# Optimization experiments

Hardware: AMD Instinct MI355X
Metric: run time of the kernel (lower is better)

The kernel has to match this reference:

```python
import jax, jax.numpy as jnp
import numpy as np

ROPE_THETA = 10000.0

def rope(x):
    # x: [B, H, T, D], D even. Standard rotate-half rotary embedding.
    T, D = x.shape[-2], x.shape[-1]
    half = D // 2
    inv_freq = 1.0 / (ROPE_THETA ** (jnp.arange(half, dtype=x.dtype) / half))
    ang = jnp.arange(T, dtype=x.dtype)[:, None] * inv_freq[None, :]  # [T, half]
    cos, sin = jnp.cos(ang), jnp.sin(ang)
    x1, x2 = x[..., :half], x[..., half:]
    return jnp.concatenate([x1 * cos - x2 * sin, x1 * sin + x2 * cos], axis=-1)


def setup_inputs() -> dict:
    key = jax.random.key(0)
    kq, kk, kv = jax.random.split(key, 3)
    shape = (2, 8, 4096, 64)  # [B, H, T, D]
    return {
        "Q": jax.random.normal(kq, shape, dtype=jnp.float32),
        "K": jax.random.normal(kk, shape, dtype=jnp.float32),
        "V": jax.random.normal(kv, shape, dtype=jnp.float32),
    }


def reference(Q, K, V):
    # Unnormalized causal linear attention with RoPE:
    #   tril(RoPE(Q) @ RoPE(K)^T, diagonal=-1) @ V
    Qr = rope(Q)
    Kr = rope(K)
    scores = jnp.einsum("bhqd,bhkd->bhqk", Qr, Kr)  # [B,H,T,T]
    T = scores.shape[-1]
    # strictly lower triangular (diagonal=-1): keep q_idx > k_idx
    mask = jnp.arange(T)[:, None] > jnp.arange(T)[None, :]
    scores = jnp.where(mask, scores, jnp.zeros((), dtype=scores.dtype))
    return jnp.einsum("bhqk,bhkd->bhqd", scores, V)
```

## Files before the change

kernel.cpp:

```cpp
#include <hip/hip_runtime.h>

#define G 16
#define T 4096
#define DD 64

typedef __attribute__((ext_vector_type(8))) short bf16x8;
typedef __attribute__((ext_vector_type(4))) short bf16x4;
typedef __attribute__((ext_vector_type(4))) float f32x4;
typedef unsigned short U16;

__device__ __forceinline__ float bf2f(U16 u) {
  union { unsigned int u; float f; } x; x.u = ((unsigned int)u) << 16; return x.f;
}
__device__ __forceinline__ U16 f2bf(float f) {
  union { float f; unsigned int u; } x; x.f = f;
  unsigned int r = x.u + 0x7FFFu + ((x.u >> 16) & 1u);
  return (U16)(r >> 16);
}

#define MFMA(a, b, c) __builtin_amdgcn_mfma_f32_16x16x32_bf16((a), (b), (c), 0, 0, 0)

#define ROPE_C 0.28782313662425575f

__global__ __launch_bounds__(256) void k_phase1(const float* __restrict__ K, const float* __restrict__ V,
                                                U16* __restrict__ Kr, U16* __restrict__ VbT,
                                                U16* __restrict__ Xu) {
  __shared__ __align__(16) U16 KrT[64][72];
  __shared__ __align__(16) U16 VT[64][72];
  int wid = blockIdx.x;
  int g = wid >> 6, b = wid & 63;
  int k0 = b * 64;
  int tid = threadIdx.x;

  int r = tid >> 2, qq = tid & 3, d0 = qq * 8;
  int t = k0 + r;
  size_t base = ((size_t)g * T + t) * DD;

  {
    const float* rp = K + base;
    float x1[8], x2[8];
    *(float4*)&x1[0] = *(const float4*)(rp + d0);
    *(float4*)&x1[4] = *(const float4*)(rp + d0 + 4);
    *(float4*)&x2[0] = *(const float4*)(rp + d0 + 32);
    *(float4*)&x2[4] = *(const float4*)(rp + d0 + 36);
    bf16x8 v1, v2;
#pragma unroll
    for (int i = 0; i < 8; ++i) {
      float invf = __expf(-(float)(d0 + i) * ROPE_C);
      float ang = (float)t * invf;
      float s, c;
      __sincosf(ang, &s, &c);
      float o1 = x1[i] * c - x2[i] * s;
      float o2 = x1[i] * s + x2[i] * c;
      U16 b1 = f2bf(o1), b2 = f2bf(o2);
      v1[i] = (short)b1; v2[i] = (short)b2;
      KrT[d0 + i][r]      = b1;
      KrT[d0 + i + 32][r] = b2;
    }
    *(bf16x8*)(Kr + base + d0)      = v1;
    *(bf16x8*)(Kr + base + d0 + 32) = v2;
  }
  {
    const float* vp = V + base;
    float y1[8], y2[8];
    *(float4*)&y1[0] = *(const float4*)(vp + d0);
    *(float4*)&y1[4] = *(const float4*)(vp + d0 + 4);
    *(float4*)&y2[0] = *(const float4*)(vp + d0 + 32);
    *(float4*)&y2[4] = *(const float4*)(vp + d0 + 36);
#pragma unroll
    for (int i = 0; i < 8; ++i) {
      VT[d0 + i][r]      = f2bf(y1[i]);
      VT[d0 + i + 32][r] = f2bf(y2[i]);
    }
  }
  __syncthreads();

  {
    int er = tid >> 2, cc = (tid & 3) * 16;
    *(bf16x8*)(VbT + ((size_t)wid << 12) + er * 64 + cc)     = *(const bf16x8*)&VT[er][cc];
    *(bf16x8*)(VbT + ((size_t)wid << 12) + er * 64 + cc + 8) = *(const bf16x8*)&VT[er][cc + 8];
  }

  int lane = tid & 63, wv = tid >> 6;
  int lr = lane & 15, lg = lane >> 4;

  bf16x8 A0 = *(const bf16x8*)&KrT[16 * wv + lr][8 * lg];
  bf16x8 A1 = *(const bf16x8*)&KrT[16 * wv + lr][8 * lg + 32];
#pragma unroll
  for (int et = 0; et < 4; ++et) {
    bf16x8 B0 = *(const bf16x8*)&VT[16 * et + lr][8 * lg];
    bf16x8 B1 = *(const bf16x8*)&VT[16 * et + lr][8 * lg + 32];
    f32x4 acc = {0.f, 0.f, 0.f, 0.f};
    acc = MFMA(A0, B0, acc);
    acc = MFMA(A1, B1, acc);
    bf16x4 st;
#pragma unroll
    for (int rr = 0; rr < 4; ++rr) st[rr] = (short)f2bf(acc[rr]);
    *(bf16x4*)(Xu + ((size_t)wid << 12) + (16 * et + lr) * 64 + 16 * wv + 4 * lg) = st;
  }
}

__global__ __launch_bounds__(256) void k_phase2c(U16* __restrict__ Xu) {
  int tau = blockIdx.x * 256 + threadIdx.x;
  int hd = tau >> 12, col = tau & 4095;
  size_t base = ((size_t)hd << 18) + col;
  U16 v[64];
#pragma unroll
  for (int i = 0; i < 64; ++i)
    v[i] = Xu[base + ((size_t)i << 12)];
  float run = 0.f;
#pragma unroll
  for (int i = 0; i < 64; ++i) {
    float f = bf2f(v[i]);
    Xu[base + ((size_t)i << 12)] = f2bf(run);
    run += f;
  }
}

__global__ __launch_bounds__(256) void k_phase3(const float* __restrict__ Q, const U16* __restrict__ Kr,
                                                const U16* __restrict__ VbT, const U16* __restrict__ Xu,
                                                float* __restrict__ Out) {
  __shared__ __align__(16) U16 SP[64][72];
  __shared__ __align__(16) U16 VT[64][72];
  __shared__ __align__(16) U16 SW[4][16][72];
  int wid = blockIdx.x;
  int g = wid >> 6, b = wid & 63;
  int k0 = b * 64;
  int tid = threadIdx.x;

  {
    int r = tid >> 2, c0 = (tid & 3) * 16;
    const U16* src = Xu + ((size_t)wid << 12) + r * 64 + c0;
    *(bf16x8*)&SP[r][c0]     = *(const bf16x8*)src;
    *(bf16x8*)&SP[r][c0 + 8] = *(const bf16x8*)(src + 8);
  }
  {
    int r = tid >> 2, c0 = (tid & 3) * 16;
    const U16* src = VbT + ((size_t)wid << 12) + r * 64 + c0;
    *(bf16x8*)&VT[r][c0]     = *(const bf16x8*)src;
    *(bf16x8*)&VT[r][c0 + 8] = *(const bf16x8*)(src + 8);
  }

  int lane = tid & 63, wv = tid >> 6;
  int lr = lane & 15, lg = lane >> 4;
  int q0 = k0 + 16 * wv;

  bf16x8 Aq0, Aq1;
  {
    int t = q0 + lr;
    const float* qrow = Q + ((size_t)g * T + t) * DD;
    float x1[8], x2[8];
    *(float4*)&x1[0] = *(const float4*)(qrow + 8 * lg);
    *(float4*)&x1[4] = *(const float4*)(qrow + 8 * lg + 4);
    *(float4*)&x2[0] = *(const float4*)(qrow + 8 * lg + 32);
    *(float4*)&x2[4] = *(const float4*)(qrow + 8 * lg + 36);
#pragma unroll
    for (int i = 0; i < 8; ++i) {
      float invf = __expf(-(float)(8 * lg + i) * ROPE_C);
      float ang = (float)t * invf;
      float s, c;
      __sincosf(ang, &s, &c);
      Aq0[i] = (short)f2bf(x1[i] * c - x2[i] * s);
      Aq1[i] = (short)f2bf(x1[i] * s + x2[i] * c);
    }
  }
  __syncthreads();

  f32x4 O[4];
#pragma unroll
  for (int et = 0; et < 4; ++et) O[et] = (f32x4){0.f, 0.f, 0.f, 0.f};

#pragma unroll
  for (int et = 0; et < 4; ++et) {
    bf16x8 B0 = *(const bf16x8*)&SP[16 * et + lr][8 * lg];
    bf16x8 B1 = *(const bf16x8*)&SP[16 * et + lr][8 * lg + 32];
    O[et] = MFMA(Aq0, B0, O[et]);
    O[et] = MFMA(Aq1, B1, O[et]);
  }

  for (int kt = 0; kt <= wv; ++kt) {
    const U16* krow = Kr + ((size_t)g * T + k0 + 16 * kt + lr) * DD;
    bf16x8 Bk0 = *(const bf16x8*)(krow + 8 * lg);
    bf16x8 Bk1 = *(const bf16x8*)(krow + 8 * lg + 32);
    f32x4 s = {0.f, 0.f, 0.f, 0.f};
    s = MFMA(Aq0, Bk0, s);
    s = MFMA(Aq1, Bk1, s);
#pragma unroll
    for (int rr = 0; rr < 4; ++rr) {
      int qi = 16 * wv + 4 * lg + rr, ki = 16 * kt + lr;
      float val = (qi > ki) ? s[rr] : 0.f;
      SW[wv][4 * lg + rr][16 * kt + lr] = f2bf(val);
    }
  }
  for (int kt = wv + 1; kt < 4; ++kt) {
#pragma unroll
    for (int rr = 0; rr < 4; ++rr)
      SW[wv][4 * lg + rr][16 * kt + lr] = 0;
  }

  bf16x8 As0 = *(const bf16x8*)&SW[wv][lr][8 * lg];
  bf16x8 As1 = *(const bf16x8*)&SW[wv][lr][8 * lg + 32];

#pragma unroll
  for (int et = 0; et < 4; ++et) {
    bf16x8 Bv0 = *(const bf16x8*)&VT[16 * et + lr][8 * lg];
    bf16x8 Bv1 = *(const bf16x8*)&VT[16 * et + lr][8 * lg + 32];
    O[et] = MFMA(As0, Bv0, O[et]);
    O[et] = MFMA(As1, Bv1, O[et]);
  }

#pragma unroll
  for (int et = 0; et < 4; ++et)
#pragma unroll
    for (int rr = 0; rr < 4; ++rr)
      __builtin_nontemporal_store(O[et][rr],
          &Out[((size_t)g * T + q0 + 4 * lg + rr) * DD + 16 * et + lr]);
}

extern "C" void kernel_launch(void* const* d_in, const int* in_sizes, int n_in,
                              void* d_out, int out_size, void* d_ws, size_t ws_size,
                              hipStream_t stream) {
  const float* Q = (const float*)d_in[0];
  const float* K = (const float*)d_in[1];
  const float* V = (const float*)d_in[2];
  float* Out = (float*)d_out;
  U16* W  = (U16*)d_ws;
  U16* Kr  = W;
  U16* VbT = W + 4194304;
  U16* Xu  = W + 8388608;
  k_phase1<<<G * 64, 256, 0, stream>>>(K, V, Kr, VbT, Xu);
  k_phase2c<<<256, 256, 0, stream>>>(Xu);
  k_phase3<<<G * 64, 256, 0, stream>>>(Q, Kr, VbT, Xu, Out);
}
```

Baseline: 29.90 us.

## Double the chunk size from 64 to 128 across all three phases

Each block now handles a 128-token chunk, processed as two 64-row halves, instead of 64 tokens, and the launch grids shrink to match. Phase 1 builds 64x64 chunk states from 128 keys. The prefix-scan kernel runs over 32 chunks instead of 64. Phase 3 computes the intra-chunk causal term as a 128-wide score tile, with the second half of the queries attending to the full first half of the keys. The aim is to cut the serial scan length and the per-chunk state traffic, at the cost of more quadratic intra-chunk MFMA work and larger LDS tiles per block.

```diff
diff --git a/kernel.cpp b/kernel.cpp
--- a/kernel.cpp
+++ b/kernel.cpp
@@ -25,92 +25,106 @@
 __global__ __launch_bounds__(256) void k_phase1(const float* __restrict__ K, const float* __restrict__ V,
                                                 U16* __restrict__ Kr, U16* __restrict__ VbT,
                                                 U16* __restrict__ Xu) {
-  __shared__ __align__(16) U16 KrT[64][72];
-  __shared__ __align__(16) U16 VT[64][72];
+  __shared__ __align__(16) U16 KrT[64][136];
+  __shared__ __align__(16) U16 VT[64][136];
   int wid = blockIdx.x;
-  int g = wid >> 6, b = wid & 63;
-  int k0 = b * 64;
+  int g = wid >> 5, j = wid & 31;
+  int k0 = j * 128;
   int tid = threadIdx.x;
-
   int r = tid >> 2, qq = tid & 3, d0 = qq * 8;
-  int t = k0 + r;
-  size_t base = ((size_t)g * T + t) * DD;
-
-  {
-    const float* rp = K + base;
-    float x1[8], x2[8];
-    *(float4*)&x1[0] = *(const float4*)(rp + d0);
-    *(float4*)&x1[4] = *(const float4*)(rp + d0 + 4);
-    *(float4*)&x2[0] = *(const float4*)(rp + d0 + 32);
-    *(float4*)&x2[4] = *(const float4*)(rp + d0 + 36);
-    bf16x8 v1, v2;
-#pragma unroll
-    for (int i = 0; i < 8; ++i) {
-      float invf = __expf(-(float)(d0 + i) * ROPE_C);
-      float ang = (float)t * invf;
-      float s, c;
-      __sincosf(ang, &s, &c);
-      float o1 = x1[i] * c - x2[i] * s;
-      float o2 = x1[i] * s + x2[i] * c;
-      U16 b1 = f2bf(o1), b2 = f2bf(o2);
-      v1[i] = (short)b1; v2[i] = (short)b2;
-      KrT[d0 + i][r]      = b1;
-      KrT[d0 + i + 32][r] = b2;
-    }
-    *(bf16x8*)(Kr + base + d0)      = v1;
-    *(bf16x8*)(Kr + base + d0 + 32) = v2;
-  }
-  {
-    const float* vp = V + base;
-    float y1[8], y2[8];
-    *(float4*)&y1[0] = *(const float4*)(vp + d0);
-    *(float4*)&y1[4] = *(const float4*)(vp + d0 + 4);
-    *(float4*)&y2[0] = *(const float4*)(vp + d0 + 32);
-    *(float4*)&y2[4] = *(const float4*)(vp + d0 + 36);
-#pragma unroll
-    for (int i = 0; i < 8; ++i) {
-      VT[d0 + i][r]      = f2bf(y1[i]);
-      VT[d0 + i + 32][r] = f2bf(y2[i]);
+
+#pragma unroll
+  for (int h = 0; h < 2; ++h) {
+    int t = k0 + 64 * h + r;
+    size_t base = ((size_t)g * T + t) * DD;
+    {
+      const float* rp = K + base;
+      float x1[8], x2[8];
+      *(float4*)&x1[0] = *(const float4*)(rp + d0);
+      *(float4*)&x1[4] = *(const float4*)(rp + d0 + 4);
+      *(float4*)&x2[0] = *(const float4*)(rp + d0 + 32);
+      *(float4*)&x2[4] = *(const float4*)(rp + d0 + 36);
+      bf16x8 v1, v2;
+#pragma unroll
+      for (int i = 0; i < 8; ++i) {
+        float invf = __expf(-(float)(d0 + i) * ROPE_C);
+        float ang = (float)t * invf;
+        float s, c;
+        __sincosf(ang, &s, &c);
+        float o1 = x1[i] * c - x2[i] * s;
+        float o2 = x1[i] * s + x2[i] * c;
+        U16 b1 = f2bf(o1), b2 = f2bf(o2);
+        v1[i] = (short)b1; v2[i] = (short)b2;
+        KrT[d0 + i][64 * h + r]      = b1;
+        KrT[d0 + i + 32][64 * h + r] = b2;
+      }
+      *(bf16x8*)(Kr + base + d0)      = v1;
+      *(bf16x8*)(Kr + base + d0 + 32) = v2;
+    }
+    {
+      const float* vp = V + base;
+      float y1[8], y2[8];
+      *(float4*)&y1[0] = *(const float4*)(vp + d0);
+      *(float4*)&y1[4] = *(const float4*)(vp + d0 + 4);
+      *(float4*)&y2[0] = *(const float4*)(vp + d0 + 32);
+      *(float4*)&y2[4] = *(const float4*)(vp + d0 + 36);
+#pragma unroll
+      for (int i = 0; i < 8; ++i) {
+        VT[d0 + i][64 * h + r]      = f2bf(y1[i]);
+        VT[d0 + i + 32][64 * h + r] = f2bf(y2[i]);
+      }
     }
   }
   __syncthreads();
 
   {
-    int er = tid >> 2, cc = (tid & 3) * 16;
-    *(bf16x8*)(VbT + ((size_t)wid << 12) + er * 64 + cc)     = *(const bf16x8*)&VT[er][cc];
-    *(bf16x8*)(VbT + ((size_t)wid << 12) + er * 64 + cc + 8) = *(const bf16x8*)&VT[er][cc + 8];
+    int er = tid >> 2, cc = (tid & 3) * 32;
+    U16* dst = VbT + ((size_t)wid << 13) + er * 128 + cc;
+    *(bf16x8*)(dst)      = *(const bf16x8*)&VT[er][cc];
+    *(bf16x8*)(dst + 8)  = *(const bf16x8*)&VT[er][cc + 8];
+    *(bf16x8*)(dst + 16) = *(const bf16x8*)&VT[er][cc + 16];
+    *(bf16x8*)(dst + 24) = *(const bf16x8*)&VT[er][cc + 24];
   }
 
   int lane = tid & 63, wv = tid >> 6;
   int lr = lane & 15, lg = lane >> 4;
 
-  bf16x8 A0 = *(const bf16x8*)&KrT[16 * wv + lr][8 * lg];
-  bf16x8 A1 = *(const bf16x8*)&KrT[16 * wv + lr][8 * lg + 32];
-#pragma unroll
-  for (int et = 0; et < 4; ++et) {
-    bf16x8 B0 = *(const bf16x8*)&VT[16 * et + lr][8 * lg];
-    bf16x8 B1 = *(const bf16x8*)&VT[16 * et + lr][8 * lg + 32];
-    f32x4 acc = {0.f, 0.f, 0.f, 0.f};
-    acc = MFMA(A0, B0, acc);
-    acc = MFMA(A1, B1, acc);
-    bf16x4 st;
-#pragma unroll
-    for (int rr = 0; rr < 4; ++rr) st[rr] = (short)f2bf(acc[rr]);
-    *(bf16x4*)(Xu + ((size_t)wid << 12) + (16 * et + lr) * 64 + 16 * wv + 4 * lg) = st;
+  {
+    bf16x8 A[2][2];
+#pragma unroll
+    for (int h = 0; h < 2; ++h) {
+      A[h][0] = *(const bf16x8*)&KrT[16 * wv + lr][64 * h + 8 * lg];
+      A[h][1] = *(const bf16x8*)&KrT[16 * wv + lr][64 * h + 8 * lg + 32];
+    }
+#pragma unroll
+    for (int et = 0; et < 4; ++et) {
+      f32x4 acc = {0.f, 0.f, 0.f, 0.f};
+#pragma unroll
+      for (int h = 0; h < 2; ++h) {
+        bf16x8 B0 = *(const bf16x8*)&VT[16 * et + lr][64 * h + 8 * lg];
+        bf16x8 B1 = *(const bf16x8*)&VT[16 * et + lr][64 * h + 8 * lg + 32];
+        acc = MFMA(A[h][0], B0, acc);
+        acc = MFMA(A[h][1], B1, acc);
+      }
+      bf16x4 st;
+#pragma unroll
+      for (int rr = 0; rr < 4; ++rr) st[rr] = (short)f2bf(acc[rr]);
+      *(bf16x4*)(Xu + ((size_t)wid << 12) + (16 * et + lr) * 64 + 16 * wv + 4 * lg) = st;
+    }
   }
 }
 
 __global__ __launch_bounds__(256) void k_phase2c(U16* __restrict__ Xu) {
   int tau = blockIdx.x * 256 + threadIdx.x;
   int hd = tau >> 12, col = tau & 4095;
-  size_t base = ((size_t)hd << 18) + col;
-  U16 v[64];
-#pragma unroll
-  for (int i = 0; i < 64; ++i)
+  size_t base = ((size_t)hd << 17) + col;
+  U16 v[32];
+#pragma unroll
+  for (int i = 0; i < 32; ++i)
     v[i] = Xu[base + ((size_t)i << 12)];
   float run = 0.f;
 #pragma unroll
-  for (int i = 0; i < 64; ++i) {
+  for (int i = 0; i < 32; ++i) {
     float f = bf2f(v[i]);
     Xu[base + ((size_t)i << 12)] = f2bf(run);
     run += f;
@@ -121,11 +135,11 @@
                                                 const U16* __restrict__ VbT, const U16* __restrict__ Xu,
                                                 float* __restrict__ Out) {
   __shared__ __align__(16) U16 SP[64][72];
-  __shared__ __align__(16) U16 VT[64][72];
-  __shared__ __align__(16) U16 SW[4][16][72];
+  __shared__ __align__(16) U16 VT[64][136];
+  __shared__ __align__(16) U16 SW[4][16][136];
   int wid = blockIdx.x;
-  int g = wid >> 6, b = wid & 63;
-  int k0 = b * 64;
+  int g = wid >> 5, j = wid & 31;
+  int k0 = j * 128;
   int tid = threadIdx.x;
 
   {
@@ -135,86 +149,117 @@
     *(bf16x8*)&SP[r][c0 + 8] = *(const bf16x8*)(src + 8);
   }
   {
-    int r = tid >> 2, c0 = (tid & 3) * 16;
-    const U16* src = VbT + ((size_t)wid << 12) + r * 64 + c0;
-    *(bf16x8*)&VT[r][c0]     = *(const bf16x8*)src;
-    *(bf16x8*)&VT[r][c0 + 8] = *(const bf16x8*)(src + 8);
-  }
+    int r = tid >> 2, cc = (tid & 3) * 32;
+    const U16* src = VbT + ((size_t)wid << 13) + r * 128 + cc;
+    *(bf16x8*)&VT[r][cc]      = *(const bf16x8*)src;
+    *(bf16x8*)&VT[r][cc + 8]  = *(const bf16x8*)(src + 8);
+    *(bf16x8*)&VT[r][cc + 16] = *(const bf16x8*)(src + 16);
+    *(bf16x8*)&VT[r][cc + 24] = *(const bf16x8*)(src + 24);
+  }
+  __syncthreads();
 
   int lane = tid & 63, wv = tid >> 6;
   int lr = lane & 15, lg = lane >> 4;
-  int q0 = k0 + 16 * wv;
-
-  bf16x8 Aq0, Aq1;
-  {
-    int t = q0 + lr;
-    const float* qrow = Q + ((size_t)g * T + t) * DD;
-    float x1[8], x2[8];
-    *(float4*)&x1[0] = *(const float4*)(qrow + 8 * lg);
-    *(float4*)&x1[4] = *(const float4*)(qrow + 8 * lg + 4);
-    *(float4*)&x2[0] = *(const float4*)(qrow + 8 * lg + 32);
-    *(float4*)&x2[4] = *(const float4*)(qrow + 8 * lg + 36);
-#pragma unroll
-    for (int i = 0; i < 8; ++i) {
-      float invf = __expf(-(float)(8 * lg + i) * ROPE_C);
-      float ang = (float)t * invf;
-      float s, c;
-      __sincosf(ang, &s, &c);
-      Aq0[i] = (short)f2bf(x1[i] * c - x2[i] * s);
-      Aq1[i] = (short)f2bf(x1[i] * s + x2[i] * c);
-    }
-  }
-  __syncthreads();
-
-  f32x4 O[4];
-#pragma unroll
-  for (int et = 0; et < 4; ++et) O[et] = (f32x4){0.f, 0.f, 0.f, 0.f};
-
-#pragma unroll
-  for (int et = 0; et < 4; ++et) {
-    bf16x8 B0 = *(const bf16x8*)&SP[16 * et + lr][8 * lg];
-    bf16x8 B1 = *(const bf16x8*)&SP[16 * et + lr][8 * lg + 32];
-    O[et] = MFMA(Aq0, B0, O[et]);
-    O[et] = MFMA(Aq1, B1, O[et]);
-  }
-
-  for (int kt = 0; kt <= wv; ++kt) {
-    const U16* krow = Kr + ((size_t)g * T + k0 + 16 * kt + lr) * DD;
-    bf16x8 Bk0 = *(const bf16x8*)(krow + 8 * lg);
-    bf16x8 Bk1 = *(const bf16x8*)(krow + 8 * lg + 32);
-    f32x4 s = {0.f, 0.f, 0.f, 0.f};
-    s = MFMA(Aq0, Bk0, s);
-    s = MFMA(Aq1, Bk1, s);
-#pragma unroll
-    for (int rr = 0; rr < 4; ++rr) {
-      int qi = 16 * wv + 4 * lg + rr, ki = 16 * kt + lr;
-      float val = (qi > ki) ? s[rr] : 0.f;
-      SW[wv][4 * lg + rr][16 * kt + lr] = f2bf(val);
-    }
-  }
-  for (int kt = wv + 1; kt < 4; ++kt) {
-#pragma unroll
-    for (int rr = 0; rr < 4; ++rr)
-      SW[wv][4 * lg + rr][16 * kt + lr] = 0;
-  }
-
-  bf16x8 As0 = *(const bf16x8*)&SW[wv][lr][8 * lg];
-  bf16x8 As1 = *(const bf16x8*)&SW[wv][lr][8 * lg + 32];
-
-#pragma unroll
-  for (int et = 0; et < 4; ++et) {
-    bf16x8 Bv0 = *(const bf16x8*)&VT[16 * et + lr][8 * lg];
-    bf16x8 Bv1 = *(const bf16x8*)&VT[16 * et + lr][8 * lg + 32];
-    O[et] = MFMA(As0, Bv0, O[et]);
-    O[et] = MFMA(As1, Bv1, O[et]);
-  }
-
-#pragma unroll
-  for (int et = 0; et < 4; ++et)
-#pragma unroll
-    for (int rr = 0; rr < 4; ++rr)
-      __builtin_nontemporal_store(O[et][rr],
-          &Out[((size_t)g * T + q0 + 4 * lg + rr) * DD + 16 * et + lr]);
+
+  f32x4 O[2][4];
+#pragma unroll
+  for (int h = 0; h < 2; ++h)
+#pragma unroll
+    for (int et = 0; et < 4; ++et) O[h][et] = (f32x4){0.f, 0.f, 0.f, 0.f};
+
+#pragma unroll
+  for (int h = 0; h < 2; ++h) {
+    int q0 = k0 + 64 * h + 16 * wv;
+    bf16x8 Aq0, Aq1;
+    {
+      int t = q0 + lr;
+      const float* qrow = Q + ((size_t)g * T + t) * DD;
+      float x1[8], x2[8];
+      *(float4*)&x1[0] = *(const float4*)(qrow + 8 * lg);
+      *(float4*)&x1[4] = *(const float4*)(qrow + 8 * lg + 4);
+      *(float4*)&x2[0] = *(const float4*)(qrow + 8 * lg + 32);
+      *(float4*)&x2[4] = *(const float4*)(qrow + 8 * lg + 36);
+#pragma unroll
+      for (int i = 0; i < 8; ++i) {
+        float invf = __expf(-(float)(8 * lg + i) * ROPE_C);
+        float ang = (float)t * invf;
+        float s, c;
+        __sincosf(ang, &s, &c);
+        Aq0[i] = (short)f2bf(x1[i] * c - x2[i] * s);
+        Aq1[i] = (short)f2bf(x1[i] * s + x2[i] * c);
+      }
+    }
+
+#pragma unroll
+    for (int et = 0; et < 4; ++et) {
+      bf16x8 B0 = *(const bf16x8*)&SP[16 * et + lr][8 * lg];
+      bf16x8 B1 = *(const bf16x8*)&SP[16 * et + lr][8 * lg + 32];
+      O[h][et] = MFMA(Aq0, B0, O[h][et]);
+      O[h][et] = MFMA(Aq1, B1, O[h][et]);
+    }
+
+    {
+      bf16x8 z = {0, 0, 0, 0, 0, 0, 0, 0};
+      *(bf16x8*)&SW[wv][lr][32 * lg]      = z;
+      *(bf16x8*)&SW[wv][lr][32 * lg + 8]  = z;
+      *(bf16x8*)&SW[wv][lr][32 * lg + 16] = z;
+      *(bf16x8*)&SW[wv][lr][32 * lg + 24] = z;
+    }
+
+    if (h == 1) {
+#pragma unroll
+      for (int kt0 = 0; kt0 < 4; ++kt0) {
+        const U16* krow = Kr + ((size_t)g * T + k0 + 16 * kt0 + lr) * DD;
+        bf16x8 Bk0 = *(const bf16x8*)(krow + 8 * lg);
+        bf16x8 Bk1 = *(const bf16x8*)(krow + 8 * lg + 32);
+        f32x4 s = {0.f, 0.f, 0.f, 0.f};
+        s = MFMA(Aq0, Bk0, s);
+        s = MFMA(Aq1, Bk1, s);
+        bf16x4 st;
+#pragma unroll
+        for (int rr = 0; rr < 4; ++rr) st[rr] = (short)f2bf(s[rr]);
+#pragma unroll
+        for (int rr = 0; rr < 4; ++rr)
+          SW[wv][4 * lg + rr][16 * kt0 + lr] = (U16)st[rr];
+      }
+    }
+
+    for (int kt = 0; kt <= wv; ++kt) {
+      const U16* krow = Kr + ((size_t)g * T + k0 + 64 * h + 16 * kt + lr) * DD;
+      bf16x8 Bk0 = *(const bf16x8*)(krow + 8 * lg);
+      bf16x8 Bk1 = *(const bf16x8*)(krow + 8 * lg + 32);
+      f32x4 s = {0.f, 0.f, 0.f, 0.f};
+      s = MFMA(Aq0, Bk0, s);
+      s = MFMA(Aq1, Bk1, s);
+#pragma unroll
+      for (int rr = 0; rr < 4; ++rr) {
+        int qi = 16 * wv + 4 * lg + rr, ki = 16 * kt + lr;
+        float val = (qi > ki) ? s[rr] : 0.f;
+        SW[wv][4 * lg + rr][64 * h + 16 * kt + lr] = f2bf(val);
+      }
+    }
+
+    int nks = (h == 0) ? 2 : 4;
+    for (int ks = 0; ks < nks; ++ks) {
+      bf16x8 As = *(const bf16x8*)&SW[wv][lr][32 * ks + 8 * lg];
+#pragma unroll
+      for (int et = 0; et < 4; ++et) {
+        bf16x8 Bv = *(const bf16x8*)&VT[16 * et + lr][32 * ks + 8 * lg];
+        O[h][et] = MFMA(As, Bv, O[h][et]);
+      }
+    }
+  }
+
+#pragma unroll
+  for (int h = 0; h < 2; ++h) {
+    int q0 = k0 + 64 * h + 16 * wv;
+#pragma unroll
+    for (int et = 0; et < 4; ++et)
+#pragma unroll
+      for (int rr = 0; rr < 4; ++rr)
+        __builtin_nontemporal_store(O[h][et][rr],
+            &Out[((size_t)g * T + q0 + 4 * lg + rr) * DD + 16 * et + lr]);
+  }
 }
 
 extern "C" void kernel_launch(void* const* d_in, const int* in_sizes, int n_in,
@@ -228,7 +273,7 @@
   U16* Kr  = W;
   U16* VbT = W + 4194304;
   U16* Xu  = W + 8388608;
-  k_phase1<<<G * 64, 256, 0, stream>>>(K, V, Kr, VbT, Xu);
+  k_phase1<<<G * 32, 256, 0, stream>>>(K, V, Kr, VbT, Xu);
   k_phase2c<<<256, 256, 0, stream>>>(Xu);
-  k_phase3<<<G * 64, 256, 0, stream>>>(Q, Kr, VbT, Xu, Out);
-}
+  k_phase3<<<G * 32, 256, 0, stream>>>(Q, Kr, VbT, Xu, Out);
+}
```

New measurement: 30.12 us. Within noise of the previous version (+0.7%).
